# Kernel tuning notes

Measured on AMD Instinct MI355X. Metric: run time of the kernel, lower is better.

## Reference

```python
import jax, jax.numpy as jnp
from jax import lax
import numpy as np

B = 512
EPS = 1e-5


def _conv(x, w, b):
    # x: [B,C,H,W], w: [O,I,3,3], stride 1, pad 1 (same spatial)
    y = lax.conv_general_dilated(x, w, window_strides=(1, 1),
                                 padding=[(1, 1), (1, 1)],
                                 dimension_numbers=('NCHW', 'OIHW', 'NCHW'))
    return y + b[None, :, None, None]


def _bn(x, g, b, m, v):
    # eval-mode batchnorm with running stats
    inv = g * lax.rsqrt(v + EPS)
    return x * inv[None, :, None, None] + (b - m * inv)[None, :, None, None]


def _maxpool2(x):
    return lax.reduce_window(x, -jnp.inf, lax.max, (1, 1, 2, 2), (1, 1, 2, 2), 'VALID')


def _block(x, w, b, g, be, m, v):
    return _maxpool2(jax.nn.relu(_bn(_conv(x, w, b), g, be, m, v)))


def setup_inputs() -> dict:
    key = jax.random.key(0)
    ks = jax.random.split(key, 12)
    n = lambda k, s: jax.random.normal(k, s, jnp.float32) * 0.05
    z = lambda s: jnp.zeros(s, jnp.float32)
    o = lambda s: jnp.ones(s, jnp.float32)
    return {
        'x': jax.random.normal(ks[0], (B, 1, 48, 48), jnp.float32),
        'conv1_w': n(ks[1], (256, 1, 3, 3)), 'conv1_b': z((256,)),
        'bn1_g': o((256,)), 'bn1_b': z((256,)), 'bn1_m': z((256,)), 'bn1_v': o((256,)),
        'conv2_w': n(ks[2], (128, 256, 3, 3)), 'conv2_b': z((128,)),
        'bn2_g': o((128,)), 'bn2_b': z((128,)), 'bn2_m': z((128,)), 'bn2_v': o((128,)),
        'conv3_w': n(ks[3], (64, 128, 3, 3)), 'conv3_b': z((64,)),
        'bn3_g': o((64,)), 'bn3_b': z((64,)), 'bn3_m': z((64,)), 'bn3_v': o((64,)),
        'fc1_w': n(ks[4], (512, 2304)), 'fc1_b': z((512,)),
        'fc2_w': n(ks[5], (256, 512)), 'fc2_b': z((256,)),
        'att_w': n(ks[6], (64, 256)), 'att_b': z((64,)),
        'fc3_w': n(ks[7], (7, 64)), 'fc3_b': z((7,)),
    }


def reference(x, conv1_w, conv1_b, bn1_g, bn1_b, bn1_m, bn1_v,
              conv2_w, conv2_b, bn2_g, bn2_b, bn2_m, bn2_v,
              conv3_w, conv3_b, bn3_g, bn3_b, bn3_m, bn3_v,
              fc1_w, fc1_b, fc2_w, fc2_b, att_w, att_b, fc3_w, fc3_b):
    out1 = _block(x, conv1_w, conv1_b, bn1_g, bn1_b, bn1_m, bn1_v)      # [B,256,24,24]
    out2 = _block(out1, conv2_w, conv2_b, bn2_g, bn2_b, bn2_m, bn2_v)   # [B,128,12,12]
    out3 = _block(out2, conv3_w, conv3_b, bn3_g, bn3_b, bn3_m, bn3_v)   # [B,64,6,6]
    b_ = out3.shape[0]
    out4 = out3.reshape(b_, -1)                                          # [B,2304]
    out5 = out4 @ fc1_w.T + fc1_b                                        # [B,512]
    out6 = out5 @ fc2_w.T + fc2_b                                        # [B,256]
    # spatial attention: query projected to channel dim of out3
    q = out6 @ att_w.T + att_b                                           # [B,64]
    scores = jnp.einsum('bchw,bc->bhw', out3, q).reshape(b_, -1)         # [B,36]
    attn = jax.nn.softmax(scores, axis=1).reshape(b_, 6, 6)
    g_mod = jnp.einsum('bchw,bhw->bc', out3, attn)                       # [B,64]
    return g_mod @ fc3_w.T + fc3_b                                       # [B,7]
```

## Files before the change

### kernel.cpp

```cpp
#include <hip/hip_runtime.h>
#include <hip/hip_bf16.h>
#include <math.h>

#define EPS_BN 1e-5f

typedef __bf16 bf16x8 __attribute__((ext_vector_type(8)));
typedef float f32x4 __attribute__((ext_vector_type(4)));
typedef float f32x2 __attribute__((ext_vector_type(2)));

__device__ __forceinline__ void gl2lds16(const void* g, void* l) {
  __builtin_amdgcn_global_load_lds(
      (const __attribute__((address_space(1))) unsigned int*)g,
      (__attribute__((address_space(3))) unsigned int*)l, 16, 0, 0);
}

__global__ __launch_bounds__(256) void k_conv1(
    const float* __restrict__ x, const float* __restrict__ w,
    const float* __restrict__ cb, const float* __restrict__ g,
    const float* __restrict__ bb, const float* __restrict__ m,
    const float* __restrict__ v, __hip_bfloat16* __restrict__ out1p,
    __hip_bfloat16* __restrict__ out2p, const float* __restrict__ W32,
    const float* __restrict__ fc1w, float* __restrict__ Wet, int n1) {
  __shared__ float xp[14 * 50];
  const int bq = blockIdx.x;
  const int t = threadIdx.x;
  if (bq >= n1) {
    int idx = (bq - n1) * 256 + t;
    int r = idx / 2304, c = idx - r * 2304;
    float s = 0.f;
    for (int k = 0; k < 512; k++)
      s = fmaf(W32[r * 512 + k], fc1w[k * 2304 + c], s);
    Wet[c * 64 + r] = s;
    return;
  }
  const int b = bq >> 2, q = bq & 3;
  __hip_bfloat16* ob = out1p + (size_t)b * (26 * 26 * 256);
  const __hip_bfloat16 z = __float2bfloat16(0.f);
  if (q == 0)
    for (int i = t; i < 26 * 256; i += 256) ob[i] = z;
  if (q == 3)
    for (int i = t; i < 26 * 256; i += 256) ob[25 * 26 * 256 + i] = z;
  for (int i = t; i < 6 * 2 * 256; i += 256) {
    int r = 1 + 6 * q + (i >> 9), side = (i >> 8) & 1, c = i & 255;
    ob[(r * 26 + side * 25) * 256 + c] = z;
  }
  {
    __hip_bfloat16* o2 = out2p + (size_t)b * (14 * 14 * 128);
    if (q == 0)
      for (int i = t; i < 14 * 128; i += 256) o2[i] = z;
    if (q == 1)
      for (int i = t; i < 14 * 128; i += 256) o2[13 * 14 * 128 + i] = z;
    if (q == 2)
      for (int i = t; i < 6 * 2 * 128; i += 256) {
        int r = 1 + (i >> 8), side = (i >> 7) & 1, c = i & 127;
        o2[(r * 14 + side * 13) * 128 + c] = z;
      }
    if (q == 3)
      for (int i = t; i < 6 * 2 * 128; i += 256) {
        int r = 7 + (i >> 8), side = (i >> 7) & 1, c = i & 127;
        o2[(r * 14 + side * 13) * 128 + c] = z;
      }
  }
  for (int i = t; i < 14 * 50; i += 256) xp[i] = 0.f;
  __syncthreads();
  const float* xb = x + (size_t)b * 2304;
  for (int i = t; i < 14 * 48; i += 256) {
    int rr = i / 48, c = i - rr * 48;
    int gr = 12 * q - 1 + rr;
    if (gr >= 0 && gr < 48) xp[rr * 50 + c + 1] = xb[gr * 48 + c];
  }
  __syncthreads();
  float wr[9];
#pragma unroll
  for (int i = 0; i < 9; i++) wr[i] = w[t * 9 + i];
  const float scale = g[t] * rsqrtf(v[t] + EPS_BN);
  const float bias = (cb[t] - m[t]) * scale + bb[t];
#pragma unroll
  for (int ohl = 0; ohl < 6; ohl++) {
    const int r0 = 2 * ohl;
    f32x2 c01[4];
#pragma unroll
    for (int r = 0; r < 4; r++) c01[r] = *(const f32x2*)&xp[(r0 + r) * 50];
#pragma unroll 4
    for (int ow = 0; ow < 24; ow++) {
      f32x2 c23[4];
#pragma unroll
      for (int r = 0; r < 4; r++)
        c23[r] = *(const f32x2*)&xp[(r0 + r) * 50 + 2 * ow + 2];
      f32x2 s2a = 0.f, s2b = 0.f;
#pragma unroll
      for (int r = 0; r < 4; r++) {
        f32x2 p0 = c01[r], p2 = c23[r];
        f32x2 p1 = {p0.y, p2.x};
        if (r <= 2) {
          s2a += p0 * wr[r * 3 + 0];
          s2a += p1 * wr[r * 3 + 1];
          s2a += p2 * wr[r * 3 + 2];
        }
        if (r >= 1) {
          s2b += p0 * wr[(r - 1) * 3 + 0];
          s2b += p1 * wr[(r - 1) * 3 + 1];
          s2b += p2 * wr[(r - 1) * 3 + 2];
        }
      }
      f32x2 b0 = s2a * scale + bias;
      f32x2 b1 = s2b * scale + bias;
      float mx = fmaxf(fmaxf(b0.x, b0.y), fmaxf(b1.x, b1.y));
      ob[((6 * q + ohl + 1) * 26 + (ow + 1)) * 256 + t] =
          __float2bfloat16(fmaxf(mx, 0.f));
#pragma unroll
      for (int r = 0; r < 4; r++) c01[r] = c23[r];
    }
  }
}

__global__ void k_prep(const float* __restrict__ c2w,
                       __hip_bfloat16* __restrict__ wt2,
                       const float* __restrict__ c3w,
                       __hip_bfloat16* __restrict__ wt3,
                       const float* __restrict__ attw,
                       const float* __restrict__ fc2w, float* __restrict__ W32,
                       const float* __restrict__ fc1b,
                       const float* __restrict__ fc2b,
                       const float* __restrict__ attb, float* __restrict__ be) {
  const int blk = blockIdx.x, tid = threadIdx.x;
  if (blk < 1152) {
    int idx = blk * 256 + tid;
    int icr = idx & 7;
    int oc = (idx >> 3) & 127;
    int rest = idx >> 10;
    int icg = rest & 31;
    int p = rest >> 5;
    wt2[idx] = __float2bfloat16(c2w[(oc * 256 + icg * 8 + icr) * 9 + p]);
  } else if (blk < 1440) {
    int idx = (blk - 1152) * 256 + tid;
    int icr = idx & 7;
    int oc = (idx >> 3) & 63;
    int rest = idx >> 9;
    int icg = rest & 15;
    int p = rest >> 4;
    wt3[idx] = __float2bfloat16(c3w[(oc * 128 + icg * 8 + icr) * 9 + p]);
  } else if (blk < 1568) {
    int idx = (blk - 1440) * 256 + tid;
    int r = idx >> 9, c = idx & 511;
    float s = 0.f;
    for (int k = 0; k < 256; k++)
      s = fmaf(attw[r * 256 + k], fc2w[k * 512 + c], s);
    W32[idx] = s;
  } else {
    __shared__ float t1[256];
    float s = fc2b[tid];
    for (int k = 0; k < 512; k++) s = fmaf(fc2w[tid * 512 + k], fc1b[k], s);
    t1[tid] = s;
    __syncthreads();
    if (tid < 64) {
      float r = attb[tid];
      for (int k = 0; k < 256; k++) r = fmaf(attw[tid * 256 + k], t1[k], r);
      be[tid] = r;
    }
  }
}

template <int HW, int IC, int OC, int NW_M, int NW_N>
__global__ __launch_bounds__(256) void k_mconv(
    const __hip_bfloat16* __restrict__ in, const __hip_bfloat16* __restrict__ wt,
    const float* __restrict__ cb, const float* __restrict__ gg,
    const float* __restrict__ bbv, const float* __restrict__ bm,
    const float* __restrict__ bv, __hip_bfloat16* __restrict__ outp) {
  constexpr int HP = HW + 2;
  constexpr int MT = NW_M * 48;
  constexpr int ROWS = MT / HW;
  constexpr int TILES = HW / ROWS;
  constexpr int WN = OC / NW_N;
  constexpr int NF = WN / 16;
  constexpr int CP = HP;
  constexpr int NCH = 6 * CP * 8;
  constexpr int NCHP = (NCH + 255) & ~255;
  constexpr int NLD = NCHP / 256;
  constexpr int NSTG = IC / 64;
  constexpr int ABUF = NCHP * 16;
  constexpr int ICG = IC / 8;
  constexpr int EPITCH = OC + 1;
  constexpr int EBYTES = 48 * EPITCH * 4;
  constexpr int SMB = (2 * ABUF) > EBYTES ? (2 * ABUF) : EBYTES;

  __shared__ __align__(16) char smraw[SMB];
  float* se = (float*)smraw;

  const int tid = threadIdx.x;
  const int wv = tid >> 6, ln = tid & 63;
  const int wm = wv >> 1, wn = wv & 1;
  const int lhi = ln >> 4, llo = ln & 15;

  const int per = gridDim.x >> 3;
  const int xcd = blockIdx.x & 7, sl = blockIdx.x >> 3;
  const int b = xcd * (per / TILES) + sl / TILES;
  const int T = sl % TILES;
  const int h0 = T * ROWS;

  const __hip_bfloat16* inb = in + (size_t)b * HP * HP * IC;

  int srcoff[NLD];
#pragma unroll
  for (int i = 0; i < NLD; i++) {
    int ci = tid + i * 256;
    if (ci >= NCH) ci = NCH - 1;
    int kgslot = ci & 7;
    int rest = ci >> 3;
    int c = rest % CP;
    int r = rest / CP;
    int kg = kgslot ^ (c & 7);
    srcoff[i] = ((h0 + r) * HP + c) * IC + kg * 8;
  }
  int spb[3][3], msk[3][3];
#pragma unroll
  for (int mt = 0; mt < 3; mt++) {
    int m = wm * 48 + mt * 16 + llo;
    int hl = m / HW, wl = m % HW;
#pragma unroll
    for (int pw = 0; pw < 3; pw++) {
      spb[mt][pw] = (hl * CP + wl + pw) * 8;
      msk[mt][pw] = (wl + pw) & 7;
    }
  }
  const __hip_bfloat16* wtb = wt + (size_t)(lhi * OC + wn * WN + llo) * 8;

  f32x4 acc[3][NF];
  const f32x4 fz = {0.f, 0.f, 0.f, 0.f};
#pragma unroll
  for (int i = 0; i < 3; i++)
#pragma unroll
    for (int j = 0; j < NF; j++) acc[i][j] = fz;

#pragma unroll
  for (int i = 0; i < NLD; i++)
    gl2lds16(inb + srcoff[i], smraw + (tid + i * 256) * 16);
  __syncthreads();

#pragma unroll
  for (int s = 0; s < NSTG; s++) {
    if (s + 1 < NSTG) {
      char* nb = smraw + ((s + 1) & 1) * ABUF;
#pragma unroll
      for (int i = 0; i < NLD; i++)
        gl2lds16(inb + srcoff[i] + (s + 1) * 64, nb + (tid + i * 256) * 16);
    }
    const char* cw = smraw + (s & 1) * ABUF;
#pragma unroll
    for (int p = 0; p < 9; p++) {
      const int ph = p / 3, pw = p % 3;
#pragma unroll
      for (int ks = 0; ks < 2; ks++) {
        const int kg = ks * 4 + lhi;
        bf16x8 bf[NF];
#pragma unroll
        for (int j = 0; j < NF; j++)
          bf[j] = *(const bf16x8*)(wtb +
                                   ((size_t)(p * ICG + s * 8 + ks * 4) * OC) *
                                       8 +
                                   j * 128);
        bf16x8 af[3];
#pragma unroll
        for (int mt = 0; mt < 3; mt++) {
          int slot = spb[mt][pw] + ph * CP * 8 + (kg ^ msk[mt][pw]);
          af[mt] = *(const bf16x8*)(cw + slot * 16);
        }
#pragma unroll
        for (int mt = 0; mt < 3; mt++)
#pragma unroll
          for (int j = 0; j < NF; j++)
            acc[mt][j] = __builtin_amdgcn_mfma_f32_16x16x32_bf16(
                af[mt], bf[j], acc[mt][j], 0, 0, 0);
      }
    }
    __syncthreads();
  }

  constexpr int PR = 48 / HW;
  constexpr int POH = PR / 2;
  constexpr int OHW = HW / 2;
  constexpr int NP = POH * OHW * OC;
#pragma unroll
  for (int a = 0; a < NW_M; a++) {
    if (a) __syncthreads();
    if (wm == a) {
#pragma unroll
      for (int j = 0; j < NF; j++) {
        int n = wn * WN + j * 16 + llo;
        float scale = gg[n] * rsqrtf(bv[n] + EPS_BN);
        float bias = (cb[n] - bm[n]) * scale + bbv[n];
#pragma unroll
        for (int mt = 0; mt < 3; mt++)
#pragma unroll
          for (int r = 0; r < 4; r++) {
            int mrow = mt * 16 + lhi * 4 + r;
            se[mrow * EPITCH + n] = fmaxf(acc[mt][j][r] * scale + bias, 0.f);
          }
      }
    }
    __syncthreads();
    for (int s = tid; s < NP; s += 256) {
      int n = s % OC;
      int ow = (s / OC) % OHW;
      int ohl = s / (OC * OHW);
      int mloc = (2 * ohl) * HW + 2 * ow;
      float x0 = se[mloc * EPITCH + n];
      float x1 = se[(mloc + 1) * EPITCH + n];
      float x2 = se[(mloc + HW) * EPITCH + n];
      float x3 = se[(mloc + HW + 1) * EPITCH + n];
      float mx = fmaxf(fmaxf(x0, x1), fmaxf(x2, x3));
      int oh = (h0 >> 1) + a * POH + ohl;
      outp[(((size_t)b * (OHW + 2) + oh + 1) * (OHW + 2) + ow + 1) * OC + n] =
          __float2bfloat16(mx);
    }
    if (a + 1 < NW_M) __syncthreads();
  }
}

__global__ __launch_bounds__(256) void k_c3attn(
    const __hip_bfloat16* __restrict__ in, const __hip_bfloat16* __restrict__ wt,
    const float* __restrict__ cb, const float* __restrict__ gg,
    const float* __restrict__ bbv, const float* __restrict__ bm,
    const float* __restrict__ bv, const float* __restrict__ Wet,
    const float* __restrict__ be, const float* __restrict__ w3,
    const float* __restrict__ b3, float* __restrict__ out, int b0) {
  constexpr int HW = 12, IC = 128, OC = 64, HP = 14, CP = 14;
  constexpr int NCH = 14 * CP * 8;
  constexpr int NCHP = (NCH + 255) & ~255;
  constexpr int NLD = NCHP / 256;
  constexpr int NSTG = 2;
  constexpr int ABUF = NCHP * 16;
  constexpr int ICG = 16;
  constexpr int EPITCH = OC + 1;

  __shared__ __align__(16) char smraw[2 * ABUF];
  __shared__ float act[64 * 37];
  __shared__ float qp[4][64];
  __shared__ float ql[64], gm[64], sc[36];
  float* se = (float*)smraw;

  const int tid = threadIdx.x;
  const int wv = tid >> 6, ln = tid & 63;
  const int lhi = ln >> 4, llo = ln & 15;
  const int b = blockIdx.x;

  const __hip_bfloat16* inb = in + (size_t)b * HP * HP * IC;

  int srcoff[NLD];
#pragma unroll
  for (int i = 0; i < NLD; i++) {
    int ci = tid + i * 256;
    if (ci >= NCH) ci = NCH - 1;
    int kgslot = ci & 7;
    int rest = ci >> 3;
    int c = rest % CP;
    int r = rest / CP;
    int kg = kgslot ^ (c & 7);
    srcoff[i] = (r * HP + c) * IC + kg * 8;
  }
  int spb[9], wlv[9];
#pragma unroll
  for (int mt = 0; mt < 9; mt++) {
    int m = mt * 16 + llo;
    int hl = m / HW, wl = m % HW;
    spb[mt] = (hl * CP + wl) * 8;
    wlv[mt] = wl;
  }
  const __hip_bfloat16* wtb = wt + (size_t)(lhi * OC + wv * 16 + llo) * 8;

  f32x4 acc[9];
  const f32x4 fz = {0.f, 0.f, 0.f, 0.f};
#pragma unroll
  for (int i = 0; i < 9; i++) acc[i] = fz;

#pragma unroll
  for (int i = 0; i < NLD; i++)
    gl2lds16(inb + srcoff[i], smraw + (tid + i * 256) * 16);
  __syncthreads();

#pragma unroll
  for (int s = 0; s < NSTG; s++) {
    if (s + 1 < NSTG) {
      char* nb = smraw + ((s + 1) & 1) * ABUF;
#pragma unroll
      for (int i = 0; i < NLD; i++)
        gl2lds16(inb + srcoff[i] + (s + 1) * 64, nb + (tid + i * 256) * 16);
    }
    const char* cw = smraw + (s & 1) * ABUF;
#pragma unroll
    for (int tt = 0; tt < 18; tt++) {
      const int p = tt >> 1, ks = tt & 1;
      const int ph = p / 3, pw = p % 3;
      const int kg = ks * 4 + lhi;
      bf16x8 bf =
          *(const bf16x8*)(wtb + ((size_t)(p * ICG + s * 8 + ks * 4) * OC) * 8);
#pragma unroll
      for (int mt = 0; mt < 9; mt++) {
        int slot = spb[mt] + (ph * CP + pw) * 8 + (kg ^ ((wlv[mt] + pw) & 7));
        bf16x8 af = *(const bf16x8*)(cw + slot * 16);
        acc[mt] = __builtin_amdgcn_mfma_f32_16x16x32_bf16(af, bf, acc[mt], 0,
                                                          0, 0);
      }
    }
    __syncthreads();
  }

  {
    const int n = wv * 16 + llo;
    const float scale = gg[n] * rsqrtf(bv[n] + EPS_BN);
    const float bias = (cb[n] - bm[n]) * scale + bbv[n];
#pragma unroll
    for (int pz = 0; pz < 3; pz++) {
      if (pz) __syncthreads();
#pragma unroll
      for (int mtl = 0; mtl < 3; mtl++)
#pragma unroll
        for (int r = 0; r < 4; r++) {
          int mrow = mtl * 16 + lhi * 4 + r;
          se[mrow * EPITCH + n] =
              fmaxf(acc[pz * 3 + mtl][r] * scale + bias, 0.f);
        }
      __syncthreads();
      for (int sI = tid; sI < 2 * 6 * 64; sI += 256) {
        int nn = sI % 64;
        int ow = (sI / 64) % 6;
        int ohl = sI / (64 * 6);
        int mloc = (2 * ohl) * HW + 2 * ow;
        float x0 = se[mloc * EPITCH + nn];
        float x1 = se[(mloc + 1) * EPITCH + nn];
        float x2 = se[(mloc + HW) * EPITCH + nn];
        float x3 = se[(mloc + HW + 1) * EPITCH + nn];
        float mx = fmaxf(fmaxf(x0, x1), fmaxf(x2, x3));
        act[nn * 37 + (pz * 2 + ohl) * 6 + ow] = mx;
      }
    }
  }
  __syncthreads();

  {
    float qpv = 0.f;
    const int n = ln;
#pragma unroll 2
    for (int c2 = wv * 16; c2 < wv * 16 + 16; c2++)
      for (int hw = 0; hw < 36; hw++)
        qpv = fmaf(act[c2 * 37 + hw], Wet[(c2 * 36 + hw) * 64 + n], qpv);
    qp[wv][n] = qpv;
  }
  __syncthreads();
  if (tid < 64)
    ql[tid] = be[tid] + qp[0][tid] + qp[1][tid] + qp[2][tid] + qp[3][tid];
  __syncthreads();
  if (wv == 0) {
    float s = -INFINITY;
    if (ln < 36) {
      float a = 0.f;
      for (int c = 0; c < 64; c++) a = fmaf(act[c * 37 + ln], ql[c], a);
      s = a;
    }
    float mx = s;
    for (int off = 32; off >= 1; off >>= 1)
      mx = fmaxf(mx, __shfl_xor(mx, off));
    float e = (ln < 36) ? expf(s - mx) : 0.f;
    float sum = e;
    for (int off = 32; off >= 1; off >>= 1) sum += __shfl_xor(sum, off);
    if (ln < 36) sc[ln] = e / sum;
  }
  __syncthreads();
  if (wv == 0) {
    float gv = 0.f;
    for (int hw = 0; hw < 36; hw++) gv = fmaf(act[ln * 37 + hw], sc[hw], gv);
    gm[ln] = gv;
  }
  __syncthreads();
  if (tid < 7) {
    float a = b3[tid];
    for (int c = 0; c < 64; c++) a = fmaf(w3[tid * 64 + c], gm[c], a);
    out[(size_t)(b0 + b) * 7 + tid] = a;
  }
}

extern "C" void kernel_launch(void* const* d_in, const int* in_sizes, int n_in,
                              void* d_out, int out_size, void* d_ws,
                              size_t ws_size, hipStream_t stream) {
  const float* x    = (const float*)d_in[0];
  const float* c1w  = (const float*)d_in[1];
  const float* c1b  = (const float*)d_in[2];
  const float* g1   = (const float*)d_in[3];
  const float* bb1  = (const float*)d_in[4];
  const float* m1   = (const float*)d_in[5];
  const float* v1   = (const float*)d_in[6];
  const float* c2w  = (const float*)d_in[7];
  const float* c2b  = (const float*)d_in[8];
  const float* g2   = (const float*)d_in[9];
  const float* bb2  = (const float*)d_in[10];
  const float* m2   = (const float*)d_in[11];
  const float* v2   = (const float*)d_in[12];
  const float* c3w  = (const float*)d_in[13];
  const float* c3b  = (const float*)d_in[14];
  const float* g3   = (const float*)d_in[15];
  const float* bb3  = (const float*)d_in[16];
  const float* m3   = (const float*)d_in[17];
  const float* v3   = (const float*)d_in[18];
  const float* fc1w = (const float*)d_in[19];
  const float* fc1b = (const float*)d_in[20];
  const float* fc2w = (const float*)d_in[21];
  const float* fc2b = (const float*)d_in[22];
  const float* attw = (const float*)d_in[23];
  const float* attb = (const float*)d_in[24];
  const float* fc3w = (const float*)d_in[25];
  const float* fc3b = (const float*)d_in[26];

  const size_t PER_CHUNK = (173056ULL + 25088ULL) * 2;
  const size_t PERSIST = 589824 + 147456 + 131072 + 589824 + 256 + 8192;
  int CH = 512;
  while (CH > 8 && (size_t)CH * PER_CHUNK + PERSIST > ws_size) CH >>= 1;
  const int NCHK = 512 / CH;

  char* base = (char*)d_ws;
  size_t off = 0;
  auto alloc = [&](size_t nbytes) -> void* {
    void* p = base + off;
    off = (off + nbytes + 255) & ~(size_t)255;
    return p;
  };
  __hip_bfloat16* out1p = (__hip_bfloat16*)alloc((size_t)CH * 173056 * 2);
  __hip_bfloat16* out2p = (__hip_bfloat16*)alloc((size_t)CH * 25088 * 2);
  __hip_bfloat16* wt2  = (__hip_bfloat16*)alloc(589824);
  __hip_bfloat16* wt3  = (__hip_bfloat16*)alloc(147456);
  float* W32           = (float*)alloc(131072);
  float* Wet           = (float*)alloc(589824);
  float* be            = (float*)alloc(256);

  k_prep<<<1569, 256, 0, stream>>>(c2w, wt2, c3w, wt3, attw, fc2w, W32, fc1b,
                                   fc2b, attb, be);

  for (int c = 0; c < NCHK; c++) {
    const float* xc = x + (size_t)c * CH * 2304;
    const int n1 = CH * 4;
    const int grid1 = n1 + (c == 0 ? 576 : 0);
    k_conv1<<<grid1, 256, 0, stream>>>(xc, c1w, c1b, g1, bb1, m1, v1, out1p,
                                       out2p, W32, fc1w, Wet, n1);
    k_mconv<24, 256, 128, 2, 2>
        <<<CH * 6, 256, 0, stream>>>(out1p, wt2, c2b, g2, bb2, m2, v2, out2p);
    k_c3attn<<<CH, 256, 0, stream>>>(out2p, wt3, c3b, g3, bb3, m3, v3, Wet, be,
                                     fc3w, fc3b, (float*)d_out, c * CH);
  }
}
```

Measured before the change: 423.8 us.

## Restructure conv2 MFMA kernel with 1x4 wave split and register-pipelined weights

Replaces the templated conv2 implicit-GEMM kernel with a specialised one. Each wave now covers all 96 output pixels (6 M-tiles) and a 32-channel slice, instead of a 2x2 wave grid. Weights are repacked so each lane does one contiguous 16-byte load, and those loads run a few steps ahead in a small register ring. The next input-stage LDS prefetch is issued mid-loop instead of at stage start. The goal is more A-fragment reuse per weight load and hidden weight-load latency, at the cost of more accumulator registers and each A fragment being read by all four waves.

```diff
diff --git a/kernel.cpp b/kernel.cpp
--- a/kernel.cpp
+++ b/kernel.cpp
@@ -127,11 +127,13 @@
   if (blk < 1152) {
     int idx = blk * 256 + tid;
     int icr = idx & 7;
-    int oc = (idx >> 3) & 127;
-    int rest = idx >> 10;
-    int icg = rest & 31;
-    int p = rest >> 5;
-    wt2[idx] = __float2bfloat16(c2w[(oc * 256 + icg * 8 + icr) * 9 + p]);
+    int lhi = (idx >> 3) & 3;
+    int oc = (idx >> 5) & 127;
+    int rest = idx >> 12;
+    int kb = rest & 7;
+    int p = rest >> 3;
+    int ic = kb * 32 + lhi * 8 + icr;
+    wt2[idx] = __float2bfloat16(c2w[(oc * 256 + ic) * 9 + p]);
   } else if (blk < 1440) {
     int idx = (blk - 1152) * 256 + tid;
     int icr = idx & 7;
@@ -161,35 +163,34 @@
   }
 }
 
-template <int HW, int IC, int OC, int NW_M, int NW_N>
-__global__ __launch_bounds__(256) void k_mconv(
+__global__ __launch_bounds__(256) void k_mconv2(
     const __hip_bfloat16* __restrict__ in, const __hip_bfloat16* __restrict__ wt,
     const float* __restrict__ cb, const float* __restrict__ gg,
     const float* __restrict__ bbv, const float* __restrict__ bm,
     const float* __restrict__ bv, __hip_bfloat16* __restrict__ outp) {
-  constexpr int HP = HW + 2;
-  constexpr int MT = NW_M * 48;
-  constexpr int ROWS = MT / HW;
-  constexpr int TILES = HW / ROWS;
-  constexpr int WN = OC / NW_N;
-  constexpr int NF = WN / 16;
-  constexpr int CP = HP;
+  constexpr int HW = 24, IC = 256, OC = 128, HP = 26, CP = 26;
+  constexpr int MTW = 6;
+  constexpr int ROWS = 4;
+  constexpr int TILES = 6;
+  constexpr int WN = 32;
+  constexpr int NF = 2;
   constexpr int NCH = 6 * CP * 8;
   constexpr int NCHP = (NCH + 255) & ~255;
   constexpr int NLD = NCHP / 256;
-  constexpr int NSTG = IC / 64;
+  constexpr int NSTG = 4;
   constexpr int ABUF = NCHP * 16;
-  constexpr int ICG = IC / 8;
+  constexpr int KG = IC / 32;
   constexpr int EPITCH = OC + 1;
   constexpr int EBYTES = 48 * EPITCH * 4;
   constexpr int SMB = (2 * ABUF) > EBYTES ? (2 * ABUF) : EBYTES;
+  constexpr int NSTEP = NSTG * 18;
+  constexpr int D = 3;
 
   __shared__ __align__(16) char smraw[SMB];
   float* se = (float*)smraw;
 
   const int tid = threadIdx.x;
-  const int wv = tid >> 6, ln = tid & 63;
-  const int wm = wv >> 1, wn = wv & 1;
+  const int wn = tid >> 6, ln = tid & 63;
   const int lhi = ln >> 4, llo = ln & 15;
 
   const int per = gridDim.x >> 3;
@@ -212,108 +213,109 @@
     int kg = kgslot ^ (c & 7);
     srcoff[i] = ((h0 + r) * HP + c) * IC + kg * 8;
   }
-  int spb[3][3], msk[3][3];
-#pragma unroll
-  for (int mt = 0; mt < 3; mt++) {
-    int m = wm * 48 + mt * 16 + llo;
+  int spb[MTW], wlv[MTW];
+#pragma unroll
+  for (int mt = 0; mt < MTW; mt++) {
+    int m = mt * 16 + llo;
     int hl = m / HW, wl = m % HW;
-#pragma unroll
-    for (int pw = 0; pw < 3; pw++) {
-      spb[mt][pw] = (hl * CP + wl + pw) * 8;
-      msk[mt][pw] = (wl + pw) & 7;
-    }
-  }
-  const __hip_bfloat16* wtb = wt + (size_t)(lhi * OC + wn * WN + llo) * 8;
-
-  f32x4 acc[3][NF];
+    spb[mt] = (hl * CP + wl) * 8;
+    wlv[mt] = wl;
+  }
+  const __hip_bfloat16* wtb = wt + (wn * WN + llo) * 32 + lhi * 8;
+
+  f32x4 acc[MTW][NF];
   const f32x4 fz = {0.f, 0.f, 0.f, 0.f};
 #pragma unroll
-  for (int i = 0; i < 3; i++)
+  for (int i = 0; i < MTW; i++)
 #pragma unroll
     for (int j = 0; j < NF; j++) acc[i][j] = fz;
 
 #pragma unroll
   for (int i = 0; i < NLD; i++)
     gl2lds16(inb + srcoff[i], smraw + (tid + i * 256) * 16);
+  bf16x8 bq[D][NF];
+#pragma unroll
+  for (int d = 0; d < D; d++) {
+    const int sg = d / 18, pg = (d % 18) >> 1, kf = d & 1;
+#pragma unroll
+    for (int j = 0; j < NF; j++)
+      bq[d][j] = *(const bf16x8*)(wtb +
+                                  (size_t)((pg * KG + sg * 2 + kf) * OC) * 32 +
+                                  j * 512);
+  }
   __syncthreads();
 
 #pragma unroll
   for (int s = 0; s < NSTG; s++) {
-    if (s + 1 < NSTG) {
-      char* nb = smraw + ((s + 1) & 1) * ABUF;
-#pragma unroll
-      for (int i = 0; i < NLD; i++)
-        gl2lds16(inb + srcoff[i] + (s + 1) * 64, nb + (tid + i * 256) * 16);
-    }
     const char* cw = smraw + (s & 1) * ABUF;
 #pragma unroll
-    for (int p = 0; p < 9; p++) {
+    for (int t = 0; t < 18; t++) {
+      const int g = s * 18 + t;
+      const int p = t >> 1, ks = t & 1;
       const int ph = p / 3, pw = p % 3;
-#pragma unroll
-      for (int ks = 0; ks < 2; ks++) {
-        const int kg = ks * 4 + lhi;
-        bf16x8 bf[NF];
+      const int kg = ks * 4 + lhi;
+#pragma unroll
+      for (int mt = 0; mt < MTW; mt++) {
+        int slot = spb[mt] + (ph * CP + pw) * 8 + (kg ^ ((wlv[mt] + pw) & 7));
+        bf16x8 af = *(const bf16x8*)(cw + slot * 16);
 #pragma unroll
         for (int j = 0; j < NF; j++)
-          bf[j] = *(const bf16x8*)(wtb +
-                                   ((size_t)(p * ICG + s * 8 + ks * 4) * OC) *
-                                       8 +
-                                   j * 128);
-        bf16x8 af[3];
-#pragma unroll
-        for (int mt = 0; mt < 3; mt++) {
-          int slot = spb[mt][pw] + ph * CP * 8 + (kg ^ msk[mt][pw]);
-          af[mt] = *(const bf16x8*)(cw + slot * 16);
+          acc[mt][j] = __builtin_amdgcn_mfma_f32_16x16x32_bf16(
+              af, bq[g % D][j], acc[mt][j], 0, 0, 0);
+      }
+      if (g + D < NSTEP) {
+        const int gf = g + D;
+        const int sg = gf / 18, pg = (gf % 18) >> 1, kf = gf & 1;
+#pragma unroll
+        for (int j = 0; j < NF; j++)
+          bq[gf % D][j] =
+              *(const bf16x8*)(wtb +
+                               (size_t)((pg * KG + sg * 2 + kf) * OC) * 32 +
+                               j * 512);
+      }
+      if (t == 13 && s + 1 < NSTG) {
+        char* nb = smraw + ((s + 1) & 1) * ABUF;
+#pragma unroll
+        for (int i = 0; i < NLD; i++)
+          gl2lds16(inb + srcoff[i] + (s + 1) * 64, nb + (tid + i * 256) * 16);
+      }
+    }
+    __syncthreads();
+  }
+
+  constexpr int OHW = HW / 2;
+  constexpr int NP = 1 * OHW * OC;
+#pragma unroll
+  for (int pz = 0; pz < 2; pz++) {
+    if (pz) __syncthreads();
+#pragma unroll
+    for (int j = 0; j < NF; j++) {
+      int n = wn * WN + j * 16 + llo;
+      float scale = gg[n] * rsqrtf(bv[n] + EPS_BN);
+      float bias = (cb[n] - bm[n]) * scale + bbv[n];
+#pragma unroll
+      for (int mtl = 0; mtl < 3; mtl++)
+#pragma unroll
+        for (int r = 0; r < 4; r++) {
+          int mrow = mtl * 16 + lhi * 4 + r;
+          se[mrow * EPITCH + n] =
+              fmaxf(acc[pz * 3 + mtl][j][r] * scale + bias, 0.f);
         }
-#pragma unroll
-        for (int mt = 0; mt < 3; mt++)
-#pragma unroll
-          for (int j = 0; j < NF; j++)
-            acc[mt][j] = __builtin_amdgcn_mfma_f32_16x16x32_bf16(
-                af[mt], bf[j], acc[mt][j], 0, 0, 0);
-      }
     }
     __syncthreads();
-  }
-
-  constexpr int PR = 48 / HW;
-  constexpr int POH = PR / 2;
-  constexpr int OHW = HW / 2;
-  constexpr int NP = POH * OHW * OC;
-#pragma unroll
-  for (int a = 0; a < NW_M; a++) {
-    if (a) __syncthreads();
-    if (wm == a) {
-#pragma unroll
-      for (int j = 0; j < NF; j++) {
-        int n = wn * WN + j * 16 + llo;
-        float scale = gg[n] * rsqrtf(bv[n] + EPS_BN);
-        float bias = (cb[n] - bm[n]) * scale + bbv[n];
-#pragma unroll
-        for (int mt = 0; mt < 3; mt++)
-#pragma unroll
-          for (int r = 0; r < 4; r++) {
-            int mrow = mt * 16 + lhi * 4 + r;
-            se[mrow * EPITCH + n] = fmaxf(acc[mt][j][r] * scale + bias, 0.f);
-          }
-      }
-    }
-    __syncthreads();
-    for (int s = tid; s < NP; s += 256) {
-      int n = s % OC;
-      int ow = (s / OC) % OHW;
-      int ohl = s / (OC * OHW);
-      int mloc = (2 * ohl) * HW + 2 * ow;
+    for (int sI = tid; sI < NP; sI += 256) {
+      int n = sI % OC;
+      int ow = (sI / OC) % OHW;
+      int mloc = 2 * ow;
       float x0 = se[mloc * EPITCH + n];
       float x1 = se[(mloc + 1) * EPITCH + n];
       float x2 = se[(mloc + HW) * EPITCH + n];
       float x3 = se[(mloc + HW + 1) * EPITCH + n];
       float mx = fmaxf(fmaxf(x0, x1), fmaxf(x2, x3));
-      int oh = (h0 >> 1) + a * POH + ohl;
-      outp[(((size_t)b * (OHW + 2) + oh + 1) * (OHW + 2) + ow + 1) * OC + n] =
+      int oh = (h0 >> 1) + pz;
+      outp[(((size_t)b * 14 + oh + 1) * 14 + ow + 1) * OC + n] =
           __float2bfloat16(mx);
     }
-    if (a + 1 < NW_M) __syncthreads();
   }
 }
 
@@ -540,8 +542,8 @@
     const int grid1 = n1 + (c == 0 ? 576 : 0);
     k_conv1<<<grid1, 256, 0, stream>>>(xc, c1w, c1b, g1, bb1, m1, v1, out1p,
                                        out2p, W32, fc1w, Wet, n1);
-    k_mconv<24, 256, 128, 2, 2>
-        <<<CH * 6, 256, 0, stream>>>(out1p, wt2, c2b, g2, bb2, m2, v2, out2p);
+    k_mconv2<<<CH * 6, 256, 0, stream>>>(out1p, wt2, c2b, g2, bb2, m2, v2,
+                                         out2p);
     k_c3attn<<<CH, 256, 0, stream>>>(out2p, wt3, c3b, g3, bb3, m3, v3, Wet, be,
                                      fc3w, fc3b, (float*)d_out, c * CH);
   }
```

After: 419.9 us. About the same (-0.9%).
